# Kernel optimization log

Measured on AMD Instinct MI355X. Metric: run time of the kernel, lower is better.

Reference implementation:

```python
import jax, jax.numpy as jnp
import numpy as np

IN_DIM = 32000   # source vocab
OUT_DIM = 32000  # target vocab
HID = 1024
MAXLEN = 32      # decode steps
B = 64
SRC_LEN = 256


def _lstm_bias(h):
    # Keras LSTM: unit_forget_bias=True -> forget-gate bias = 1, rest 0. Gate order i,f,g,o.
    return jnp.concatenate([jnp.zeros(h), jnp.ones(h), jnp.zeros(2 * h)])


def setup_inputs() -> dict:
    key = jax.random.key(0)
    ks = jax.random.split(key, 12)
    g = lambda k, shape, s=0.02: (jax.random.normal(k, shape, jnp.float32) * s)
    return {
        "source": jax.random.randint(ks[0], (B, SRC_LEN), 0, IN_DIM, jnp.int32),
        "enc_emb": g(ks[1], (IN_DIM, HID)),
        "enc_K": g(ks[2], (HID, 4 * HID)),
        "enc_R": g(ks[3], (HID, 4 * HID)),
        "enc_b": _lstm_bias(HID),
        "dec_emb": g(ks[4], (OUT_DIM, HID)),
        "dec_K": g(ks[5], (HID, 4 * HID)),
        "dec_R": g(ks[6], (HID, 4 * HID)),
        "dec_b": _lstm_bias(HID),
        "W_a": g(ks[7], (HID, HID)),
        "W_c": g(ks[8], (2 * HID, HID)),
        "b_c": jnp.zeros(HID, jnp.float32),
        "W_out": g(ks[9], (HID, OUT_DIM)),
        "b_out": jnp.zeros(OUT_DIM, jnp.float32),
    }


def _lstm_cell(x, h, c, K, R, b):
    z = x @ K + h @ R + b
    i, f, g, o = jnp.split(z, 4, axis=-1)
    c = jax.nn.sigmoid(f) * c + jax.nn.sigmoid(i) * jnp.tanh(g)
    h = jax.nn.sigmoid(o) * jnp.tanh(c)
    return h, c


def reference(source, enc_emb, enc_K, enc_R, enc_b,
              dec_emb, dec_K, dec_R, dec_b,
              W_a, W_c, b_c, W_out, b_out):
    bsz = source.shape[0]
    hid = enc_K.shape[0]

    # ----- Encoder (mask_zero=True: skip state update where source==0) -----
    xe = enc_emb[source]                      # [B,T,H]
    mask = source > 0                         # [B,T]

    def enc_step(carry, xm):
        h, c = carry
        x, m = xm                             # x [B,H], m [B]
        hn, cn = _lstm_cell(x, h, c, enc_K, enc_R, enc_b)
        m = m[:, None]
        return (jnp.where(m, hn, h), jnp.where(m, cn, c)), jnp.where(m, hn, h)

    h0 = jnp.zeros((bsz, hid), xe.dtype)
    (he, ce), hs_t = jax.lax.scan(enc_step, (h0, h0),
                                  (xe.transpose(1, 0, 2), mask.T))
    hs = hs_t.transpose(1, 0, 2)              # [B,T,H] encoder states

    # ----- Decoder loop (greedy argmax feedback) -----
    hsW = hs @ W_a                            # [B,T,H], precomputed attention keys
    amask = mask[:, None, :].astype(hs.dtype)  # [B,1,T]

    def dec_step(carry, _):
        y, h, c = carry                       # y [B] int32
        x = dec_emb[y]                        # [B,H]
        hn, cn = _lstm_cell(x, h, c, dec_K, dec_R, dec_b)
        ht = hn[:, None, :]                   # [B,1,H]
        # Luong attention with source mask (exp -> mask -> normalize, as in source)
        sc = jnp.einsum('bqh,bkh->bqk', ht, hsW)        # [B,1,T]
        sc = jnp.exp(sc - sc.max(-1, keepdims=True)) * amask
        a = sc / sc.sum(-1, keepdims=True)
        ctx = jnp.einsum('bqk,bkh->bqh', a, hs)          # [B,1,H]
        ah = jnp.tanh(jnp.concatenate([ctx, ht], -1) @ W_c + b_c)
        prob = jax.nn.softmax(ah @ W_out + b_out, axis=-1)[:, 0, :]  # [B,V]
        yn = jnp.argmax(prob, axis=-1).astype(jnp.int32)
        return (yn, hn, cn), prob

    y0 = jnp.ones((bsz,), jnp.int32)          # start token = 1 (tf.ones)
    _, outs = jax.lax.scan(dec_step, (y0, he, ce), None, length=MAXLEN)
    return outs.transpose(1, 0, 2)            # [B, MAXLEN, OUT_DIM]
```

## Files before the change

### kernel.cpp

```cpp
#include <hip/hip_runtime.h>
#include <hip/hip_bf16.h>

typedef __hip_bfloat16 bf16;
typedef short bf8v __attribute__((ext_vector_type(8)));
typedef float f32x4 __attribute__((ext_vector_type(4)));

#define DEVINL __device__ __forceinline__
#define MFMA16(a, b, c) __builtin_amdgcn_mfma_f32_16x16x32_bf16((a), (b), (c), 0, 0, 0)

DEVINL float us2f(unsigned short u) { unsigned v = ((unsigned)u) << 16; return __uint_as_float(v); }
DEVINL float b2f(bf16 x) { return __bfloat162float(x); }
DEVINL bf16 f2b(float x) { return __float2bfloat16(x); }
DEVINL float sigf(float x) { return 1.0f / (1.0f + expf(-x)); }
DEVINL unsigned short f2bu(float f) { bf16 h = __float2bfloat16(f); return *(unsigned short*)&h; }

DEVINL void gload16(const void* g, void* l) {
  __builtin_amdgcn_global_load_lds((const __attribute__((address_space(1))) void*)g,
                                   (__attribute__((address_space(3))) void*)l, 16, 0, 0);
}

DEVINL unsigned ald(const unsigned* p) {
  return __hip_atomic_load(p, __ATOMIC_RELAXED, __HIP_MEMORY_SCOPE_AGENT);
}
DEVINL void ast(unsigned* p, unsigned v) {
  __hip_atomic_store(p, v, __ATOMIC_RELAXED, __HIP_MEMORY_SCOPE_AGENT);
}
DEVINL float aldf(const float* p) { unsigned u = ald((const unsigned*)p); return __uint_as_float(u); }
DEVINL void astf(float* p, float v) { ast((unsigned*)p, __float_as_uint(v)); }

DEVINL void gridbar2(unsigned* bars, unsigned lgen) {
  __syncthreads();
  if (threadIdx.x == 0) {
    unsigned s = lgen & 1;
    unsigned g = blockIdx.x >> 5;
    unsigned* grp = bars + (g * 2 + s) * 16;
    unsigned* top = bars + (16 + s) * 16;
    unsigned* gen = bars + 288;
    unsigned t = __hip_atomic_fetch_add(grp, 1u, __ATOMIC_RELAXED, __HIP_MEMORY_SCOPE_AGENT);
    if (t == 31u) {
      ast(grp, 0u);
      unsigned tt = __hip_atomic_fetch_add(top, 1u, __ATOMIC_RELAXED, __HIP_MEMORY_SCOPE_AGENT);
      if (tt == 7u) {
        ast(top, 0u);
        asm volatile("s_waitcnt vmcnt(0)");
        ast(gen, lgen + 1u);
      }
    }
    while (ald(gen) <= lgen) __builtin_amdgcn_s_sleep(4);
  }
  __syncthreads();
}

DEVINL void bar64(unsigned* b, unsigned lgen, int lid) {
  __syncthreads();
  if (threadIdx.x == 0) {
    unsigned s = lgen & 1;
    unsigned* grp = b + (((unsigned)(lid >> 5) & 1u) * 2 + s) * 16;
    unsigned* top = b + (4 + s) * 16;
    unsigned* gen = b + 96;
    unsigned t = __hip_atomic_fetch_add(grp, 1u, __ATOMIC_RELAXED, __HIP_MEMORY_SCOPE_AGENT);
    if (t == 31u) {
      ast(grp, 0u);
      unsigned tt = __hip_atomic_fetch_add(top, 1u, __ATOMIC_RELAXED, __HIP_MEMORY_SCOPE_AGENT);
      if (tt == 1u) {
        ast(top, 0u);
        asm volatile("s_waitcnt vmcnt(0)");
        ast(gen, lgen + 1u);
      }
    }
    while (ald(gen) <= lgen) __builtin_amdgcn_s_sleep(2);
  }
  __syncthreads();
}

#define OKPT_H  ((size_t)0)
#define OKPT_L  ((size_t)8388608)
#define ORPT_H  ((size_t)16777216)
#define ORPT_L  ((size_t)25165824)
#define OXE_H   ((size_t)35651584)
#define OXE_L   ((size_t)69206016)
#define OHSF5   ((size_t)35651584)
#define XCH     ((size_t)136314880)
#define OHPK_E0 (XCH + 0)
#define OHPK_E1 (XCH + 262144)
#define OHPK_D0 (XCH + 524288)
#define OCBUF5  (XCH + 1048576)
#define OAHPK   (XCH + 1310720)
#define ORSUM5  (XCH + 1572864)
#define ORMAX5  (XCH + 1638400)
#define ORIDX5  (XCH + 1769472)
#define OPSUM5  (XCH + 1900544)
#define OBARS5  (XCH + 1901568)
#define OXK_L5  ((size_t)138412032)
#define OWCT_H  ((size_t)0)
#define OWCT_L  ((size_t)4194304)
#define OPCTX5  ((size_t)8388608)
#define OQBUF   ORPT_H
#define OWOT5   ((size_t)138412032)
#define OKRTH5  ((size_t)203948032)
#define OKRTL5  ((size_t)220725248)

#define DELTA   1e-4f

#define D_LH   0
#define D_LL   32768
#define D_ZS   65536
#define D_KBH  83968
#define D_KBL  116736
#define D4_A   0
#define D4_W   16384
#define D4_E   49152
#define D_QL   0
#define D_PSC  4096
#define D_EK   8448
#define D_PC4  8704
#define D_ZS3  0
#define D_PSC2 0
#define D_GMX  4352
#define D_CCN  8512
#define D_CAND 8576
#define D_YL   149504
#define D_INV  149568
#define D_RT   149632

__global__ void ed_zero_v7(float4* p, int n) {
  int i = blockIdx.x * 256 + threadIdx.x;
  if (i < n) p[i] = make_float4(0.f, 0.f, 0.f, 0.f);
}

__global__ void ed_transpose_v7(const float* __restrict__ in, bf16* __restrict__ out,
                                int R, int C, int ostride, int ooff, int perm) {
  __shared__ float tile[32][33];
  int c0 = blockIdx.x * 32, r0 = blockIdx.y * 32;
  int tx = threadIdx.x & 31, ty0 = threadIdx.x >> 5;
#pragma unroll
  for (int i = 0; i < 4; i++) {
    int ty = ty0 + i * 8;
    tile[ty][tx] = in[(size_t)(r0 + ty) * C + c0 + tx];
  }
  __syncthreads();
#pragma unroll
  for (int i = 0; i < 4; i++) {
    int ty = ty0 + i * 8;
    int c = c0 + ty;
    int oc = perm ? ((c & 1023) * 4 + (c >> 10)) : c;
    out[(size_t)oc * ostride + ooff + r0 + tx] = f2b(tile[tx][ty]);
  }
}

__global__ void ed_transpose_split_v7(const float* __restrict__ in, bf16* __restrict__ oh,
                                      bf16* __restrict__ ol, int R, int C, int ostride,
                                      int ooff, int perm) {
  __shared__ float tile[32][33];
  int c0 = blockIdx.x * 32, r0 = blockIdx.y * 32;
  int tx = threadIdx.x & 31, ty0 = threadIdx.x >> 5;
#pragma unroll
  for (int i = 0; i < 4; i++) {
    int ty = ty0 + i * 8;
    tile[ty][tx] = in[(size_t)(r0 + ty) * C + c0 + tx];
  }
  __syncthreads();
#pragma unroll
  for (int i = 0; i < 4; i++) {
    int ty = ty0 + i * 8;
    int c = c0 + ty;
    int oc = perm ? ((c & 1023) * 4 + (c >> 10)) : c;
    float v = tile[tx][ty];
    bf16 hh = f2b(v);
    size_t o = (size_t)oc * ostride + ooff + r0 + tx;
    oh[o] = hh;
    ol[o] = f2b(v - b2f(hh));
  }
}

__global__ void ed_gather_split_v7(const int* __restrict__ src, const float* __restrict__ emb,
                                   bf16* __restrict__ xh, bf16* __restrict__ xl) {
  int bid = blockIdx.x;
  int t = bid >> 6, b = bid & 63;
  int tok = src[b * 256 + t];
  const float* rowp = emb + (size_t)tok * 1024;
  int i = threadIdx.x * 4;
  float4 v = *(const float4*)(rowp + i);
  bf16 h0 = f2b(v.x), h1 = f2b(v.y), h2 = f2b(v.z), h3 = f2b(v.w);
  ushort4 oh, ol;
  oh.x = *(unsigned short*)&h0; oh.y = *(unsigned short*)&h1;
  oh.z = *(unsigned short*)&h2; oh.w = *(unsigned short*)&h3;
  ol.x = f2bu(v.x - b2f(h0)); ol.y = f2bu(v.y - b2f(h1));
  ol.z = f2bu(v.z - b2f(h2)); ol.w = f2bu(v.w - b2f(h3));
  *(ushort4*)(xh + (size_t)bid * 1024 + i) = oh;
  *(ushort4*)(xl + (size_t)bid * 1024 + i) = ol;
}

__global__ __launch_bounds__(256, 2) void ed_gemm3_v7(
    const bf16* __restrict__ Ah, const bf16* __restrict__ Al,
    const bf16* __restrict__ Bh, const bf16* __restrict__ Bl,
    bf16* __restrict__ Ch, bf16* __restrict__ Cl, int M, int N, int K) {
  __shared__ __align__(16) bf16 Ash[128 * 32];
  __shared__ __align__(16) bf16 Asl[128 * 32];
  __shared__ __align__(16) bf16 Bsh[128 * 32];
  __shared__ __align__(16) bf16 Bsl[128 * 32];
  int m0 = blockIdx.y * 128, n0 = blockIdx.x * 128;
  int tid = threadIdx.x, w = tid >> 6, l = tid & 63;
  int wm = w >> 1, wn = w & 1;
  int lr = l & 15, lq = l >> 4;
  f32x4 acc[4][4] = {};
  for (int k0 = 0; k0 < K; k0 += 32) {
    __syncthreads();
#pragma unroll
    for (int j = 0; j < 2; j++) {
      int o = (w * 2 + j) * 1024 + l * 16;
      int rrow = o >> 6, kk = (o & 63) >> 1;
      gload16(Ah + (size_t)(m0 + rrow) * K + k0 + kk, (char*)Ash + (w * 2 + j) * 1024);
      gload16(Al + (size_t)(m0 + rrow) * K + k0 + kk, (char*)Asl + (w * 2 + j) * 1024);
      gload16(Bh + (size_t)(n0 + rrow) * K + k0 + kk, (char*)Bsh + (w * 2 + j) * 1024);
      gload16(Bl + (size_t)(n0 + rrow) * K + k0 + kk, (char*)Bsl + (w * 2 + j) * 1024);
    }
    __syncthreads();
#pragma unroll
    for (int mi = 0; mi < 4; mi++) {
      bf8v a_h = *(const bf8v*)(Ash + (wm * 64 + mi * 16 + lr) * 32 + lq * 8);
      bf8v a_l = *(const bf8v*)(Asl + (wm * 64 + mi * 16 + lr) * 32 + lq * 8);
#pragma unroll
      for (int ni = 0; ni < 4; ni++) {
        bf8v b_h = *(const bf8v*)(Bsh + (wn * 64 + ni * 16 + lr) * 32 + lq * 8);
        bf8v b_l = *(const bf8v*)(Bsl + (wn * 64 + ni * 16 + lr) * 32 + lq * 8);
        acc[mi][ni] = MFMA16(a_h, b_h, acc[mi][ni]);
        acc[mi][ni] = MFMA16(a_h, b_l, acc[mi][ni]);
        acc[mi][ni] = MFMA16(a_l, b_h, acc[mi][ni]);
      }
    }
  }
#pragma unroll
  for (int mi = 0; mi < 4; mi++)
#pragma unroll
    for (int ni = 0; ni < 4; ni++)
#pragma unroll
      for (int r = 0; r < 4; r++) {
        float v = acc[mi][ni][r];
        bf16 hh = f2b(v);
        size_t idx = (size_t)(m0 + wm * 64 + mi * 16 + lq * 4 + r) * N + n0 + wn * 64 + ni * 16 + lr;
        Ch[idx] = hh;
        Cl[idx] = f2b(v - b2f(hh));
      }
}

__global__ __launch_bounds__(1024, 4) void ed_enc_v7(
    const int* __restrict__ src, const bf16* __restrict__ Rh, const bf16* __restrict__ Rl,
    const bf16* __restrict__ Xh, const bf16* __restrict__ Xl, const float* __restrict__ enc_b,
    unsigned* hpk0, unsigned* hpk1, float* __restrict__ cbuf,
    float* __restrict__ hsf, unsigned* barsE) {
  extern __shared__ char sm[];
  bf16* lh = (bf16*)sm;
  bf16* ll = (bf16*)(sm + 32768);
  float* zs = (float*)(sm + 65536);
  float* xkf = (float*)(sm + 82944);
  int bid = blockIdx.x, tid = threadIdx.x;
  int bg = bid >> 6, cg = bid & 63, lid = bid & 63;
  unsigned* barL = barsE + bg * 128;
  int wv = tid >> 6, l = tid & 63, lr = l & 15, lq = l >> 4;
  int kq = wv >> 2, cs = wv & 3;
  int srow = tid >> 6, sj0 = (tid & 63) * 16;
  int grow = tid >> 4, gul = tid & 15;
  bf8v Rh_[8], Rl_[8];
  {
    const bf16* bh = Rh + (size_t)(cg * 64 + cs * 16 + lr) * 1024 + kq * 256 + lq * 8;
    const bf16* bl = Rl + (size_t)(cg * 64 + cs * 16 + lr) * 1024 + kq * 256 + lq * 8;
#pragma unroll
    for (int i = 0; i < 8; i++) {
      Rh_[i] = *(const bf8v*)(bh + i * 32);
      Rl_[i] = *(const bf8v*)(bl + i * 32);
    }
  }
  float bi[4];
  float c_ = 0.f;
  if (tid < 256) {
#pragma unroll
    for (int g = 0; g < 4; g++) {
      int colp = cg * 64 + gul * 4 + g;
      bi[g] = enc_b[(colp & 3) * 1024 + (colp >> 2)];
    }
  }
  unsigned *hc = hpk0, *hn = hpk1;
  unsigned lgen = 0;
  for (int t = 0; t < 256; t++) {
    {
      const unsigned* hrow = hc + (size_t)(bg * 16 + srow) * 1024 + sj0;
      unsigned u[16];
#pragma unroll
      for (int j = 0; j < 16; j++) u[j] = ald(hrow + j);
      int r8 = (srow & 7) << 3;
#pragma unroll
      for (int j = 0; j < 16; j += 2) {
        int es = (sj0 + j) ^ r8;
        *(unsigned*)((char*)lh + srow * 2048 + es * 2) = (u[j] >> 16) | (u[j + 1] & 0xffff0000u);
        *(unsigned*)((char*)ll + srow * 2048 + es * 2) = (u[j] & 0xffffu) | (u[j + 1] << 16);
      }
    }
    {
      int xr = tid >> 6, xc = tid & 63;
      size_t xi = ((size_t)t * 64 + bg * 16 + xr) * 4096 + cg * 64 + xc;
      unsigned short xh = __builtin_nontemporal_load((const unsigned short*)(Xh + xi));
      unsigned short xl = __builtin_nontemporal_load((const unsigned short*)(Xl + xi));
      xkf[xr * 64 + xc] = us2f(xh) + us2f(xl);
    }
    __syncthreads();
    {
      f32x4 acc = {0.f, 0.f, 0.f, 0.f};
      int r8 = (lr & 7) << 3;
#pragma unroll
      for (int i = 0; i < 8; i++) {
        int e0 = kq * 256 + i * 32 + lq * 8;
        int es = e0 ^ r8;
        bf8v a_h = *(const bf8v*)((char*)lh + lr * 2048 + es * 2);
        bf8v a_l = *(const bf8v*)((char*)ll + lr * 2048 + es * 2);
        acc = MFMA16(a_h, Rh_[i], acc);
        acc = MFMA16(a_h, Rl_[i], acc);
        acc = MFMA16(a_l, Rh_[i], acc);
        acc = MFMA16(a_l, Rl_[i], acc);
      }
#pragma unroll
      for (int r = 0; r < 4; r++) zs[(kq * 16 + lq * 4 + r) * 68 + cs * 16 + lr] = acc[r];
    }
    __syncthreads();
    if (tid < 256) {
      int b_ = bg * 16 + grow, u = cg * 16 + gul;
      float zz[4];
#pragma unroll
      for (int g = 0; g < 4; g++) {
        int cc = gul * 4 + g;
        zz[g] = zs[(0 + grow) * 68 + cc] + zs[(16 + grow) * 68 + cc] +
                zs[(32 + grow) * 68 + cc] + zs[(48 + grow) * 68 + cc] +
                xkf[grow * 64 + cc] + bi[g];
      }
      float iv = sigf(zz[0]), fv = sigf(zz[1]), gv = tanhf(zz[2]), ov = sigf(zz[3]);
      float cn = fv * c_ + iv * gv;
      float hnv = ov * tanhf(cn);
      bool m = src[b_ * 256 + t] > 0;
      int es = u ^ ((grow & 7) << 3);
      float hold = b2f(*(const bf16*)((char*)lh + grow * 2048 + es * 2)) +
                   b2f(*(const bf16*)((char*)ll + grow * 2048 + es * 2));
      float hv = m ? hnv : hold;
      c_ = m ? cn : c_;
      unsigned short uh = f2bu(hv);
      unsigned pkv = ((unsigned)uh << 16) | (unsigned)f2bu(hv - us2f(uh));
      ast(hn + (size_t)b_ * 1024 + u, pkv);
      hsf[((size_t)t * 64 + b_) * 1024 + u] = hv;
    }
    bar64(barL, lgen, lid);
    lgen++;
    unsigned* tp = hc; hc = hn; hn = tp;
  }
  if (tid < 256) cbuf[(size_t)(bg * 16 + grow) * 1024 + cg * 16 + gul] = c_;
}

DEVINL void dec_lstm7(int bg, int cgl, int tid, char* sm,
                      const unsigned* hc, unsigned* hn,
                      const float* __restrict__ dec_emb,
                      const bf16* __restrict__ Kh, const bf16* __restrict__ Kl,
                      const float* __restrict__ dec_b, float& c_) {
  bf16* lh = (bf16*)(sm + D_LH);
  bf16* ll = (bf16*)(sm + D_LL);
  {
    int srow = tid >> 6, sl = tid & 63;
    const unsigned* hrow = hc + (size_t)(bg * 16 + srow) * 1024 + sl * 16;
    unsigned u[16];
#pragma unroll
    for (int j = 0; j < 16; j++) u[j] = ald(hrow + j);
    uint4 ha, hb, la, lb;
    ha.x = (u[0] >> 16) | (u[1] & 0xffff0000u);  ha.y = (u[2] >> 16) | (u[3] & 0xffff0000u);
    ha.z = (u[4] >> 16) | (u[5] & 0xffff0000u);  ha.w = (u[6] >> 16) | (u[7] & 0xffff0000u);
    hb.x = (u[8] >> 16) | (u[9] & 0xffff0000u);  hb.y = (u[10] >> 16) | (u[11] & 0xffff0000u);
    hb.z = (u[12] >> 16) | (u[13] & 0xffff0000u); hb.w = (u[14] >> 16) | (u[15] & 0xffff0000u);
    la.x = (u[0] & 0xffffu) | (u[1] << 16);  la.y = (u[2] & 0xffffu) | (u[3] << 16);
    la.z = (u[4] & 0xffffu) | (u[5] << 16);  la.w = (u[6] & 0xffffu) | (u[7] << 16);
    lb.x = (u[8] & 0xffffu) | (u[9] << 16);  lb.y = (u[10] & 0xffffu) | (u[11] << 16);
    lb.z = (u[12] & 0xffffu) | (u[13] << 16); lb.w = (u[14] & 0xffffu) | (u[15] << 16);
    int swz = (srow & 7) << 4;
    char* rbh = (char*)lh + srow * 2048;
    char* rbl = (char*)ll + srow * 2048;
    *(uint4*)(rbh + ((sl * 32) ^ swz)) = ha;
    *(uint4*)(rbh + ((sl * 32 + 16) ^ swz)) = hb;
    *(uint4*)(rbl + ((sl * 32) ^ swz)) = la;
    *(uint4*)(rbl + ((sl * 32 + 16) ^ swz)) = lb;
  }
  int wv = tid >> 6, l = tid & 63, lr = l & 15, lq = l >> 4;
  int kg2 = wv >> 2, cs = wv & 3;
  bf16* kbh = (bf16*)(sm + D_KBH);
  bf16* kbl = (bf16*)(sm + D_KBL);
  const int* y_l = (const int*)(sm + D_YL);
  float* zs = (float*)(sm + D_ZS);
  f32x4 acc = {0.f, 0.f, 0.f, 0.f};
  int colB = cs * 16 + lr;
  int bswz = (colB & 7) << 4;
  int aswz = (lr & 7) << 4;
  for (int c = 0; c < 8; c++) {
    __syncthreads();
#pragma unroll
    for (int r = 0; r < 2; r++) {
      int i = wv * 128 + r * 64 + l;
      int col = i >> 5, j = i & 31;
      size_t se = (size_t)(cgl * 64 + col) * 2048 + c * 256 + ((size_t)(j ^ (col & 7)) << 3);
      gload16(Kh + se, (char*)kbh + wv * 2048 + r * 1024);
      gload16(Kl + se, (char*)kbl + wv * 2048 + r * 1024);
    }
    __syncthreads();
#pragma unroll
    for (int s = 0; s < 2; s++) {
      int kl = kg2 * 64 + s * 32 + lq * 8;
      bf8v b_h = *(const bf8v*)((char*)kbh + colB * 512 + ((kl * 2) ^ bswz));
      bf8v b_l = *(const bf8v*)((char*)kbl + colB * 512 + ((kl * 2) ^ bswz));
      int gk = c * 256 + kl;
      bf8v a_h, a_l;
      if (gk < 1024) {
        const float* xr = dec_emb + (size_t)y_l[lr] * 1024 + gk;
        float4 v0 = *(const float4*)xr;
        float4 v1 = *(const float4*)(xr + 4);
        float vs[8] = {v0.x, v0.y, v0.z, v0.w, v1.x, v1.y, v1.z, v1.w};
#pragma unroll
        for (int e = 0; e < 8; e++) {
          unsigned short uh = f2bu(vs[e]);
          a_h[e] = (short)uh;
          a_l[e] = (short)f2bu(vs[e] - us2f(uh));
        }
      } else {
        int hk = gk - 1024;
        a_h = *(const bf8v*)((char*)lh + lr * 2048 + ((hk * 2) ^ aswz));
        a_l = *(const bf8v*)((char*)ll + lr * 2048 + ((hk * 2) ^ aswz));
      }
      acc = MFMA16(a_h, b_h, acc);
      acc = MFMA16(a_h, b_l, acc);
      acc = MFMA16(a_l, b_h, acc);
      acc = MFMA16(a_l, b_l, acc);
    }
  }
#pragma unroll
  for (int r = 0; r < 4; r++) zs[(kg2 * 16 + lq * 4 + r) * 68 + cs * 16 + lr] = acc[r];
  __syncthreads();
  if (tid < 256) {
    int grow = tid >> 4, gul = tid & 15;
    int b_ = bg * 16 + grow;
    float zz[4];
#pragma unroll
    for (int g = 0; g < 4; g++) {
      int cc = gul * 4 + g;
      int colp = cgl * 64 + cc;
      float v = zs[(0 + grow) * 68 + cc] + zs[(16 + grow) * 68 + cc] +
                zs[(32 + grow) * 68 + cc] + zs[(48 + grow) * 68 + cc];
      zz[g] = v + dec_b[(colp & 3) * 1024 + (colp >> 2)];
    }
    float iv = sigf(zz[0]), fv = sigf(zz[1]), gv = tanhf(zz[2]), ov = sigf(zz[3]);
    float cn = fv * c_ + iv * gv;
    c_ = cn;
    float hv = ov * tanhf(cn);
    unsigned short uh = f2bu(hv);
    unsigned pkv = ((unsigned)uh << 16) | (unsigned)f2bu(hv - us2f(uh));
    ast(hn + (size_t)b_ * 1024 + cgl * 16 + gul, pkv);
  }
}

__global__ __launch_bounds__(1024, 4) void ed_dec_v7(
    const int* __restrict__ src,
    const bf16* __restrict__ KRh, const bf16* __restrict__ KRl, const float* __restrict__ dec_b,
    const bf16* __restrict__ WcTh, const bf16* __restrict__ WcTl, const float* __restrict__ b_cp,
    const bf16* __restrict__ WoTh, const float* __restrict__ b_op,
    const float* __restrict__ Wout_f32, const float* __restrict__ dec_emb,
    const float* __restrict__ W_a, float* __restrict__ qbuf,
    const float* __restrict__ hsf,
    unsigned* hpkA, unsigned* hpkB, float* __restrict__ cbuf,
    float* __restrict__ pctx, float* __restrict__ psum, unsigned* ahpk,
    float* __restrict__ rowsum, float* __restrict__ rmax, int* __restrict__ ridx,
    float* __restrict__ out, unsigned* barsG, unsigned* barsL) {
  extern __shared__ char sm[];
  int bid = blockIdx.x, tid = threadIdx.x;
  int bg = bid >> 6, cgl = bid & 63, lid = bid & 63;
  unsigned* barL = barsL + bg * 128;
  int wv = tid >> 6, l = tid & 63, lr = l & 15, lq = l >> 4;
  float c_ = 0.f;
  if (tid < 256) c_ = cbuf[(size_t)(bg * 16 + (tid >> 4)) * 1024 + cgl * 16 + (tid & 15)];
  unsigned *hc = hpkA, *hn = hpkB;
  unsigned lgenL = 0, lgenG = 0;

  if (tid < 16) ((int*)(sm + D_YL))[tid] = 1;
  __syncthreads();
  dec_lstm7(bg, cgl, tid, sm, hc, hn, dec_emb, KRh, KRl, dec_b, c_);
  bar64(barL, lgenL, lid); lgenL++;
  { unsigned* tp = hc; hc = hn; hn = tp; }

  for (int st = 0; st < 32; st++) {
    if (cgl < 16) {
      int colb = cgl * 64;
      int kq = wv >> 2, nq = wv & 3;
      float* zs = (float*)(sm + D_ZS);
      f32x4 acc = {0.f, 0.f, 0.f, 0.f};
      const unsigned* hrow = hc + (size_t)(bg * 16 + lr) * 1024;
      const float* warow = W_a + (size_t)(colb + nq * 16 + lr) * 1024;
#pragma unroll
      for (int i = 0; i < 8; i++) {
        int k = kq * 256 + i * 32 + lq * 8;
        bf8v a, b;
        const unsigned* hp = hrow + k;
#pragma unroll
        for (int e = 0; e < 8; e++) a[e] = (short)(ald(hp + e) >> 16);
        const float* wp = warow + k;
        float4 w0 = *(const float4*)wp;
        float4 w1 = *(const float4*)(wp + 4);
        b[0] = (short)f2bu(w0.x); b[1] = (short)f2bu(w0.y);
        b[2] = (short)f2bu(w0.z); b[3] = (short)f2bu(w0.w);
        b[4] = (short)f2bu(w1.x); b[5] = (short)f2bu(w1.y);
        b[6] = (short)f2bu(w1.z); b[7] = (short)f2bu(w1.w);
        acc = MFMA16(a, b, acc);
      }
#pragma unroll
      for (int r = 0; r < 4; r++) zs[(kq * 16 + lq * 4 + r) * 68 + nq * 16 + lr] = acc[r];
      __syncthreads();
      {
        int mrow = tid >> 6, col = tid & 63;
        float v = zs[(0 + mrow) * 68 + col] + zs[(16 + mrow) * 68 + col] +
                  zs[(32 + mrow) * 68 + col] + zs[(48 + mrow) * 68 + col];
        astf(qbuf + (size_t)(bg * 16 + mrow) * 1024 + colb + col, v);
      }
    }
    bar64(barL, lgenL, lid); lgenL++;
    {
      int b_ = bid >> 2, kg = bid & 3;
      float* q_l = (float*)(sm + D_QL);
      q_l[tid] = aldf(qbuf + (size_t)b_ * 1024 + tid);
      __syncthreads();
      float* psc = (float*)(sm + D_PSC);
      {
        int kl = tid >> 4, qq = tid & 15;
        const float* hrow = hsf + ((size_t)(kg * 64 + kl) * 64 + b_) * 1024;
        float p = 0.f;
#pragma unroll 4
        for (int j = 0; j < 16; j++) {
          int e0 = j * 64 + qq * 4;
          float4 hv = *(const float4*)(hrow + e0);
          p += hv.x * q_l[e0] + hv.y * q_l[e0 + 1] + hv.z * q_l[e0 + 2] + hv.w * q_l[e0 + 3];
        }
        psc[kl * 17 + qq] = p;
      }
      __syncthreads();
      float* ek = (float*)(sm + D_EK);
      if (tid < 64) {
        float sc = 0.f;
#pragma unroll
        for (int q = 0; q < 16; q++) sc += psc[tid * 17 + q];
        ek[tid] = (src[b_ * 256 + kg * 64 + tid] > 0) ? expf(sc) : 0.f;
      }
      __syncthreads();
      float* pc4 = (float*)(sm + D_PC4);
      {
        int cq = tid & 255, kc = tid >> 8;
        float a0 = 0.f, a1 = 0.f, a2 = 0.f, a3 = 0.f;
#pragma unroll 4
        for (int j = 0; j < 16; j++) {
          float e = ek[kc * 16 + j];
          const float* hr = hsf + ((size_t)(kg * 64 + kc * 16 + j) * 64 + b_) * 1024 + cq * 4;
          float4 uv = *(const float4*)hr;
          a0 += e * uv.x; a1 += e * uv.y; a2 += e * uv.z; a3 += e * uv.w;
        }
        pc4[kc * 1024 + cq * 4 + 0] = a0;
        pc4[kc * 1024 + cq * 4 + 1] = a1;
        pc4[kc * 1024 + cq * 4 + 2] = a2;
        pc4[kc * 1024 + cq * 4 + 3] = a3;
      }
      __syncthreads();
      {
        float v = pc4[tid] + pc4[1024 + tid] + pc4[2048 + tid] + pc4[3072 + tid];
        astf(pctx + ((size_t)kg * 64 + b_) * 1024 + tid, v);
      }
      if (tid == 0) {
        float* ek2 = (float*)(sm + D_EK);
        float s_ = 0.f;
        for (int i2 = 0; i2 < 64; i2++) s_ += ek2[i2];
        astf(psum + kg * 64 + b_, s_);
      }
    }
    bar64(barL, lgenL, lid); lgenL++;
    {
      float* inv_l = (float*)(sm + D_INV);
      if (tid < 16) {
        int rb = bg * 16 + tid;
        float sg = aldf(psum + rb) + aldf(psum + 64 + rb) +
                   aldf(psum + 128 + rb) + aldf(psum + 192 + rb);
        inv_l[tid] = 1.0f / sg;
      }
      __syncthreads();
      float* zs3 = (float*)(sm + D_ZS3);
      {
        int kq = wv;
        f32x4 acc = {0.f, 0.f, 0.f, 0.f};
        const bf16* bh = WcTh + (size_t)(cgl * 16 + lr) * 2048;
        const bf16* bl = WcTl + (size_t)(cgl * 16 + lr) * 2048;
        float inv = inv_l[lr];
#pragma unroll
        for (int i = 0; i < 4; i++) {
          int k = kq * 128 + i * 32 + lq * 8;
          bf8v a_h, a_l;
          if (k < 1024) {
            const float* p0 = pctx + (size_t)(bg * 16 + lr) * 1024 + k;
#pragma unroll
            for (int e = 0; e < 8; e++) {
              float v = (aldf(p0 + e) + aldf(p0 + 65536 + e) +
                         aldf(p0 + 131072 + e) + aldf(p0 + 196608 + e)) * inv;
              unsigned short uh = f2bu(v);
              a_h[e] = (short)uh;
              a_l[e] = (short)f2bu(v - us2f(uh));
            }
          } else {
            const unsigned* hp = hc + (size_t)(bg * 16 + lr) * 1024 + (k - 1024);
#pragma unroll
            for (int e = 0; e < 8; e++) {
              unsigned u = ald(hp + e);
              a_h[e] = (short)(u >> 16);
              a_l[e] = (short)(u & 0xffffu);
            }
          }
          bf8v b_h = *(const bf8v*)(bh + k);
          bf8v b_l = *(const bf8v*)(bl + k);
          acc = MFMA16(a_h, b_h, acc); acc = MFMA16(a_h, b_l, acc);
          acc = MFMA16(a_l, b_h, acc); acc = MFMA16(a_l, b_l, acc);
        }
#pragma unroll
        for (int r = 0; r < 4; r++) zs3[(kq * 16 + lq * 4 + r) * 17 + lr] = acc[r];
      }
      __syncthreads();
      if (tid < 256) {
        int grow = tid >> 4, gcol = tid & 15;
        float v = 0.f;
#pragma unroll
        for (int q = 0; q < 16; q++) v += zs3[(q * 16 + grow) * 17 + gcol];
        v += b_cp[cgl * 16 + gcol];
        float ahv = tanhf(v);
        unsigned short uh = f2bu(ahv);
        unsigned pkv = ((unsigned)uh << 16) | (unsigned)f2bu(ahv - us2f(uh));
        ast(ahpk + (size_t)(bg * 16 + grow) * 1024 + cgl * 16 + gcol, pkv);
      }
    }
    gridbar2(barsG, lgenG); lgenG++;
    {
      int base = bid * 125;
      bf16* abuf = (bf16*)(sm + D4_A);
      bf16* wbuf = (bf16*)(sm + D4_W);
      int rg = wv >> 2, cpair = wv & 3;
      f32x4 acc0 = {0.f, 0.f, 0.f, 0.f}, acc1 = {0.f, 0.f, 0.f, 0.f};
      for (int kc = 0; kc < 8; kc++) {
        int k0 = kc * 128;
        __syncthreads();
        {
          int row = tid >> 4, l16 = tid & 15;
          const unsigned* ap = ahpk + (size_t)row * 1024 + k0 + l16 * 8;
          unsigned u0 = ald(ap), u1 = ald(ap + 1), u2 = ald(ap + 2), u3 = ald(ap + 3);
          unsigned u4 = ald(ap + 4), u5 = ald(ap + 5), u6 = ald(ap + 6), u7 = ald(ap + 7);
          uint4 hv;
          hv.x = (u0 >> 16) | (u1 & 0xffff0000u);
          hv.y = (u2 >> 16) | (u3 & 0xffff0000u);
          hv.z = (u4 >> 16) | (u5 & 0xffff0000u);
          hv.w = (u6 >> 16) | (u7 & 0xffff0000u);
          *(uint4*)((char*)abuf + row * 256 + ((l16 * 16) ^ ((row & 7) << 4))) = hv;
        }
#pragma unroll
        for (int r = 0; r < 2; r++) {
          int i = wv * 128 + r * 64 + l;
          int col = i >> 4, j = i & 15;
          int ccol = col < 125 ? col : 124;
          size_t se = (size_t)(base + ccol) * 1024 + k0 + ((size_t)(j ^ (col & 7)) << 3);
          gload16(WoTh + se, (char*)wbuf + wv * 2048 + r * 1024);
        }
        __syncthreads();
#pragma unroll
        for (int s = 0; s < 4; s++) {
          int kl = s * 32 + lq * 8;
          int ar = rg * 16 + lr;
          bf8v a = *(const bf8v*)((char*)abuf + ar * 256 + ((kl * 2) ^ ((ar & 7) << 4)));
          int c0 = cpair * 32 + lr, c1 = c0 + 16;
          bf8v b0 = *(const bf8v*)((char*)wbuf + c0 * 256 + ((kl * 2) ^ ((c0 & 7) << 4)));
          bf8v b1 = *(const bf8v*)((char*)wbuf + c1 * 256 + ((kl * 2) ^ ((c1 & 7) << 4)));
          acc0 = MFMA16(a, b0, acc0);
          acc1 = MFMA16(a, b1, acc1);
        }
      }
      __syncthreads();
      float* e = (float*)(sm + D4_E);
      {
        int cl0 = cpair * 32 + lr;
        if (cl0 < 125) {
#pragma unroll
          for (int r = 0; r < 4; r++)
            e[(rg * 16 + lq * 4 + r) * 129 + cl0] = acc0[r] + b_op[base + cl0];
        }
        int cl1 = cpair * 32 + 16 + lr;
        if (cl1 < 125) {
#pragma unroll
          for (int r = 0; r < 4; r++)
            e[(rg * 16 + lq * 4 + r) * 129 + cl1] = acc1[r] + b_op[base + cl1];
        }
      }
      __syncthreads();
      if (tid < 64) {
        float sm_ = 0.f, v1 = -1e30f, v2 = -1e30f;
        int i1 = 0, i2 = 0;
        for (int c2 = 0; c2 < 125; c2++) {
          float v = e[tid * 129 + c2];
          sm_ += expf(v);
          if (v > v1) { v2 = v1; i2 = i1; v1 = v; i1 = base + c2; }
          else if (v > v2) { v2 = v; i2 = base + c2; }
        }
        astf(rowsum + bid * 64 + tid, sm_);
        astf(rmax + (bid * 64 + tid) * 2 + 0, v1);
        ast((unsigned*)ridx + (bid * 64 + tid) * 2 + 0, (unsigned)i1);
        astf(rmax + (bid * 64 + tid) * 2 + 1, v2);
        ast((unsigned*)ridx + (bid * 64 + tid) * 2 + 1, (unsigned)i2);
      }
    }
    gridbar2(barsG, lgenG); lgenG++;
    {
      float* psc2 = (float*)(sm + D_PSC2);
      {
        int rr = tid & 63, pp = tid >> 6;
        float s_ = 0.f;
#pragma unroll 4
        for (int cu = pp * 16; cu < pp * 16 + 16; cu++) s_ += aldf(rowsum + cu * 64 + rr);
        psc2[rr * 17 + pp] = s_;
      }
      __syncthreads();
      float* rt = (float*)(sm + D_RT);
      if (tid < 64) {
        float s_ = 0.f;
#pragma unroll
        for (int p2 = 0; p2 < 16; p2++) s_ += psc2[tid * 17 + p2];
        rt[tid] = s_;
      }
      __syncthreads();
      float* e = (float*)(sm + D4_E);
      {
        int base = bid * 125;
        for (int i = tid; i < 8000; i += 1024) {
          int r_ = i / 125, c2 = i - r_ * 125;
          float pv = expf(e[r_ * 129 + c2]) / rt[r_];
          __builtin_nontemporal_store(pv, out + ((size_t)r_ * 32 + st) * 32000 + base + c2);
        }
      }
      if (st < 31) {
        float* gmx = (float*)(sm + D_GMX);
        int* ccnt = (int*)(sm + D_CCN);
        int* cand = (int*)(sm + D_CAND);
        int* y_l = (int*)(sm + D_YL);
        int r16 = tid & 15, ch = tid >> 4;
        int rowg = bg * 16 + r16;
        float vloc[8]; int iloc[8];
        {
          float m_ = -1e30f;
#pragma unroll
          for (int ee = 0; ee < 8; ee++) {
            int ent = ch * 8 + ee;
            vloc[ee] = aldf(rmax + ((size_t)(ent >> 1) * 64 + rowg) * 2 + (ent & 1));
            iloc[ee] = (int)ald((const unsigned*)ridx + ((size_t)(ent >> 1) * 64 + rowg) * 2 + (ent & 1));
            m_ = fmaxf(m_, vloc[ee]);
          }
          gmx[r16 * 65 + ch] = m_;
        }
        if (tid < 16) ccnt[tid] = 0;
        __syncthreads();
        if (tid < 16) {
          float g_ = -1e30f;
#pragma unroll
          for (int j = 0; j < 64; j++) g_ = fmaxf(g_, gmx[tid * 65 + j]);
          gmx[tid * 65 + 64] = g_;
        }
        __syncthreads();
        {
          float thr = gmx[r16 * 65 + 64] - DELTA;
#pragma unroll
          for (int ee = 0; ee < 8; ee++) {
            if (vloc[ee] >= thr) {
              int slot = atomicAdd(&ccnt[r16], 1);
              if (slot < 8) cand[r16 * 8 + slot] = iloc[ee];
            }
          }
        }
        __syncthreads();
        {
          int row2 = wv;
          int rowg2 = bg * 16 + row2;
          int cnt = ccnt[row2]; if (cnt > 8) cnt = 8;
          double bv = -1e30; int bi_ = 0x7fffffff;
          for (int ci = 0; ci < cnt; ci++) {
            int c = cand[row2 * 8 + ci];
            double s_ = 0.0;
            for (int k = l; k < 1024; k += 64) {
              unsigned u = ald(ahpk + (size_t)rowg2 * 1024 + k);
              float av = us2f((unsigned short)(u >> 16)) + us2f((unsigned short)(u & 0xffffu));
              float wv_ = __builtin_nontemporal_load(Wout_f32 + (size_t)k * 32000 + c);
              s_ += (double)av * (double)wv_;
            }
#pragma unroll
            for (int off = 32; off > 0; off >>= 1) s_ += __shfl_down(s_, off);
            if (l == 0) {
              s_ += (double)b_op[c];
              if (s_ > bv || (s_ == bv && c < bi_)) { bv = s_; bi_ = c; }
            }
          }
          if (l == 0) y_l[row2] = bi_;
        }
        __syncthreads();
        dec_lstm7(bg, cgl, tid, sm, hc, hn, dec_emb, KRh, KRl, dec_b, c_);
      }
    }
    bar64(barL, lgenL, lid); lgenL++;
    { unsigned* tp = hc; hc = hn; hn = tp; }
  }
}

extern "C" void kernel_launch(void* const* d_in, const int* in_sizes, int n_in,
                              void* d_out, int out_size, void* d_ws, size_t ws_size,
                              hipStream_t stream) {
  (void)in_sizes; (void)n_in; (void)out_size; (void)ws_size;
  const int*   src     = (const int*)  d_in[0];
  const float* enc_emb = (const float*)d_in[1];
  const float* enc_K   = (const float*)d_in[2];
  const float* enc_R   = (const float*)d_in[3];
  const float* enc_b   = (const float*)d_in[4];
  const float* dec_emb = (const float*)d_in[5];
  const float* dec_K   = (const float*)d_in[6];
  const float* dec_R   = (const float*)d_in[7];
  const float* dec_b   = (const float*)d_in[8];
  const float* W_a     = (const float*)d_in[9];
  const float* W_c     = (const float*)d_in[10];
  const float* b_c     = (const float*)d_in[11];
  const float* W_out   = (const float*)d_in[12];
  const float* b_out   = (const float*)d_in[13];
  char* ws = (char*)d_ws;

  hipFuncSetAttribute((const void*)ed_enc_v7, hipFuncAttributeMaxDynamicSharedMemorySize, 163840);
  hipFuncSetAttribute((const void*)ed_dec_v7, hipFuncAttributeMaxDynamicSharedMemorySize, 163840);

  bf16* KpTh = (bf16*)(ws + OKPT_H);
  bf16* KpTl = (bf16*)(ws + OKPT_L);
  bf16* RpTh = (bf16*)(ws + ORPT_H);
  bf16* RpTl = (bf16*)(ws + ORPT_L);
  bf16* xeh  = (bf16*)(ws + OXE_H);
  bf16* xel  = (bf16*)(ws + OXE_L);
  float* hsf = (float*)(ws + OHSF5);
  unsigned* hpkE0 = (unsigned*)(ws + OHPK_E0);
  unsigned* hpkE1 = (unsigned*)(ws + OHPK_E1);
  unsigned* hpkD0 = (unsigned*)(ws + OHPK_D0);
  float* cbuf = (float*)(ws + OCBUF5);
  unsigned* ahpk = (unsigned*)(ws + OAHPK);
  float* rsum = (float*)(ws + ORSUM5);
  float* rmaxp = (float*)(ws + ORMAX5);
  int*  ridxp = (int*)(ws + ORIDX5);
  float* psum = (float*)(ws + OPSUM5);
  unsigned* barsE = (unsigned*)(ws + OBARS5);
  unsigned* barsG = (unsigned*)(ws + OBARS5 + 4096);
  unsigned* barsL = (unsigned*)(ws + OBARS5 + 8192);
  bf16* XkL  = (bf16*)(ws + OXK_L5);
  bf16* XkH  = (bf16*)d_out;
  bf16* WcTh = (bf16*)(ws + OWCT_H);
  bf16* WcTl = (bf16*)(ws + OWCT_L);
  float* pctx = (float*)(ws + OPCTX5);
  float* qbuf = (float*)(ws + OQBUF);
  bf16* WoTh = (bf16*)(ws + OWOT5);
  bf16* KRTh = (bf16*)(ws + OKRTH5);
  bf16* KRTl = (bf16*)(ws + OKRTL5);

  ed_zero_v7<<<512, 256, 0, stream>>>((float4*)(ws + XCH), 131072);
  ed_transpose_split_v7<<<dim3(128, 32), 256, 0, stream>>>(enc_K, KpTh, KpTl, 1024, 4096, 1024, 0, 1);
  ed_transpose_split_v7<<<dim3(128, 32), 256, 0, stream>>>(enc_R, RpTh, RpTl, 1024, 4096, 1024, 0, 1);
  ed_gather_split_v7<<<16384, 256, 0, stream>>>(src, enc_emb, xeh, xel);
  ed_gemm3_v7<<<dim3(32, 128), 256, 0, stream>>>(xeh, xel, KpTh, KpTl, XkH, XkL, 16384, 4096, 1024);
  ed_transpose_split_v7<<<dim3(32, 64), 256, 0, stream>>>(W_c, WcTh, WcTl, 2048, 1024, 2048, 0, 0);
  ed_enc_v7<<<256, 1024, 87040, stream>>>(src, RpTh, RpTl, XkH, XkL, enc_b,
                                          hpkE0, hpkE1, cbuf, hsf, barsE);
  ed_transpose_v7<<<dim3(1000, 32), 256, 0, stream>>>(W_out, WoTh, 1024, 32000, 1024, 0, 0);
  ed_transpose_split_v7<<<dim3(128, 32), 256, 0, stream>>>(dec_K, KRTh, KRTl, 1024, 4096, 2048, 0, 1);
  ed_transpose_split_v7<<<dim3(128, 32), 256, 0, stream>>>(dec_R, KRTh, KRTl, 1024, 4096, 2048, 1024, 1);
  ed_dec_v7<<<256, 1024, 150528, stream>>>(src, KRTh, KRTl, dec_b, WcTh, WcTl, b_c,
                                           WoTh, b_out, W_out, dec_emb, W_a, qbuf, hsf,
                                           hpkE0, hpkD0, cbuf, pctx, psum, ahpk,
                                           rsum, rmaxp, ridxp, (float*)d_out, barsG, barsL);
}
```

Measured before the change: 14.43 ms.

## Restructure decoder attention, argmax reduction, and pre-convert W_a to bf16

```diff
diff --git a/kernel.cpp b/kernel.cpp
--- a/kernel.cpp
+++ b/kernel.cpp
@@ -91,11 +91,13 @@
 #define ORIDX5  (XCH + 1769472)
 #define OPSUM5  (XCH + 1900544)
 #define OBARS5  (XCH + 1901568)
+#define OYBUF   (XCH + 1917952)
 #define OXK_L5  ((size_t)138412032)
 #define OWCT_H  ((size_t)0)
 #define OWCT_L  ((size_t)4194304)
 #define OPCTX5  ((size_t)8388608)
 #define OQBUF   ORPT_H
+#define OWAB    (ORPT_H + 262144)
 #define OWOT5   ((size_t)138412032)
 #define OKRTH5  ((size_t)203948032)
 #define OKRTL5  ((size_t)220725248)
@@ -110,25 +112,36 @@
 #define D4_A   0
 #define D4_W   16384
 #define D4_E   49152
-#define D_QL   0
-#define D_PSC  4096
-#define D_EK   8448
-#define D_PC4  8704
+#define D_WA   0
+#define D_ES   65536
 #define D_ZS3  0
 #define D_PSC2 0
-#define D_GMX  4352
-#define D_CCN  8512
-#define D_CAND 8576
+#define D_RV   0
+#define D_RR   2048
+#define D_CCN  4096
+#define D_CAND 4160
+#define D_RS   4224
+#define D_RC   4352
 #define D_YL   149504
 #define D_INV  149568
 #define D_RT   149632
 
-__global__ void ed_zero_v7(float4* p, int n) {
+__global__ void ed_zero_v8(float4* p, int n) {
   int i = blockIdx.x * 256 + threadIdx.x;
   if (i < n) p[i] = make_float4(0.f, 0.f, 0.f, 0.f);
 }
 
-__global__ void ed_transpose_v7(const float* __restrict__ in, bf16* __restrict__ out,
+__global__ void ed_cvt_v8(const float* __restrict__ in, bf16* __restrict__ out, int n) {
+  int i = (blockIdx.x * 256 + threadIdx.x) * 4;
+  if (i + 3 < n) {
+    float4 v = *(const float4*)(in + i);
+    ushort4 o;
+    o.x = f2bu(v.x); o.y = f2bu(v.y); o.z = f2bu(v.z); o.w = f2bu(v.w);
+    *(ushort4*)(out + i) = o;
+  }
+}
+
+__global__ void ed_transpose_v8(const float* __restrict__ in, bf16* __restrict__ out,
                                 int R, int C, int ostride, int ooff, int perm) {
   __shared__ float tile[32][33];
   int c0 = blockIdx.x * 32, r0 = blockIdx.y * 32;
@@ -148,7 +161,7 @@
   }
 }
 
-__global__ void ed_transpose_split_v7(const float* __restrict__ in, bf16* __restrict__ oh,
+__global__ void ed_transpose_split_v8(const float* __restrict__ in, bf16* __restrict__ oh,
                                       bf16* __restrict__ ol, int R, int C, int ostride,
                                       int ooff, int perm) {
   __shared__ float tile[32][33];
@@ -173,7 +186,7 @@
   }
 }
 
-__global__ void ed_gather_split_v7(const int* __restrict__ src, const float* __restrict__ emb,
+__global__ void ed_gather_split_v8(const int* __restrict__ src, const float* __restrict__ emb,
                                    bf16* __restrict__ xh, bf16* __restrict__ xl) {
   int bid = blockIdx.x;
   int t = bid >> 6, b = bid & 63;
@@ -191,7 +204,7 @@
   *(ushort4*)(xl + (size_t)bid * 1024 + i) = ol;
 }
 
-__global__ __launch_bounds__(256, 2) void ed_gemm3_v7(
+__global__ __launch_bounds__(256, 2) void ed_gemm3_v8(
     const bf16* __restrict__ Ah, const bf16* __restrict__ Al,
     const bf16* __restrict__ Bh, const bf16* __restrict__ Bl,
     bf16* __restrict__ Ch, bf16* __restrict__ Cl, int M, int N, int K) {
@@ -244,7 +257,7 @@
       }
 }
 
-__global__ __launch_bounds__(1024, 4) void ed_enc_v7(
+__global__ __launch_bounds__(1024, 4) void ed_enc_v8(
     const int* __restrict__ src, const bf16* __restrict__ Rh, const bf16* __restrict__ Rl,
     const bf16* __restrict__ Xh, const bf16* __restrict__ Xl, const float* __restrict__ enc_b,
     unsigned* hpk0, unsigned* hpk1, float* __restrict__ cbuf,
@@ -353,7 +366,7 @@
   if (tid < 256) cbuf[(size_t)(bg * 16 + grow) * 1024 + cg * 16 + gul] = c_;
 }
 
-DEVINL void dec_lstm7(int bg, int cgl, int tid, char* sm,
+DEVINL void dec_lstm8(int bg, int cgl, int tid, char* sm,
                       const unsigned* hc, unsigned* hn,
                       const float* __restrict__ dec_emb,
                       const bf16* __restrict__ Kh, const bf16* __restrict__ Kl,
@@ -458,18 +471,18 @@
   }
 }
 
-__global__ __launch_bounds__(1024, 4) void ed_dec_v7(
+__global__ __launch_bounds__(1024, 4) void ed_dec_v8(
     const int* __restrict__ src,
     const bf16* __restrict__ KRh, const bf16* __restrict__ KRl, const float* __restrict__ dec_b,
     const bf16* __restrict__ WcTh, const bf16* __restrict__ WcTl, const float* __restrict__ b_cp,
     const bf16* __restrict__ WoTh, const float* __restrict__ b_op,
     const float* __restrict__ Wout_f32, const float* __restrict__ dec_emb,
-    const float* __restrict__ W_a, float* __restrict__ qbuf,
+    const bf16* __restrict__ WaB, float* __restrict__ qbuf,
     const float* __restrict__ hsf,
     unsigned* hpkA, unsigned* hpkB, float* __restrict__ cbuf,
     float* __restrict__ pctx, float* __restrict__ psum, unsigned* ahpk,
     float* __restrict__ rowsum, float* __restrict__ rmax, int* __restrict__ ridx,
-    float* __restrict__ out, unsigned* barsG, unsigned* barsL) {
+    unsigned* ybuf, float* __restrict__ out, unsigned* barsG, unsigned* barsL) {
   extern __shared__ char sm[];
   int bid = blockIdx.x, tid = threadIdx.x;
   int bg = bid >> 6, cgl = bid & 63, lid = bid & 63;
@@ -482,7 +495,7 @@
 
   if (tid < 16) ((int*)(sm + D_YL))[tid] = 1;
   __syncthreads();
-  dec_lstm7(bg, cgl, tid, sm, hc, hn, dec_emb, KRh, KRl, dec_b, c_);
+  dec_lstm8(bg, cgl, tid, sm, hc, hn, dec_emb, KRh, KRl, dec_b, c_);
   bar64(barL, lgenL, lid); lgenL++;
   { unsigned* tp = hc; hc = hn; hn = tp; }
 
@@ -493,21 +506,15 @@
       float* zs = (float*)(sm + D_ZS);
       f32x4 acc = {0.f, 0.f, 0.f, 0.f};
       const unsigned* hrow = hc + (size_t)(bg * 16 + lr) * 1024;
-      const float* warow = W_a + (size_t)(colb + nq * 16 + lr) * 1024;
+      const bf16* warow = WaB + (size_t)(colb + nq * 16 + lr) * 1024;
 #pragma unroll
       for (int i = 0; i < 8; i++) {
         int k = kq * 256 + i * 32 + lq * 8;
-        bf8v a, b;
+        bf8v a;
         const unsigned* hp = hrow + k;
 #pragma unroll
         for (int e = 0; e < 8; e++) a[e] = (short)(ald(hp + e) >> 16);
-        const float* wp = warow + k;
-        float4 w0 = *(const float4*)wp;
-        float4 w1 = *(const float4*)(wp + 4);
-        b[0] = (short)f2bu(w0.x); b[1] = (short)f2bu(w0.y);
-        b[2] = (short)f2bu(w0.z); b[3] = (short)f2bu(w0.w);
-        b[4] = (short)f2bu(w1.x); b[5] = (short)f2bu(w1.y);
-        b[6] = (short)f2bu(w1.z); b[7] = (short)f2bu(w1.w);
+        bf8v b = *(const bf8v*)(warow + k);
         acc = MFMA16(a, b, acc);
       }
 #pragma unroll
@@ -523,56 +530,55 @@
     bar64(barL, lgenL, lid); lgenL++;
     {
       int b_ = bid >> 2, kg = bid & 3;
-      float* q_l = (float*)(sm + D_QL);
-      q_l[tid] = aldf(qbuf + (size_t)b_ * 1024 + tid);
-      __syncthreads();
-      float* psc = (float*)(sm + D_PSC);
+      float* wacc = (float*)(sm + D_WA);
+      float* es = (float*)(sm + D_ES);
+      float qr[16];
       {
-        int kl = tid >> 4, qq = tid & 15;
-        const float* hrow = hsf + ((size_t)(kg * 64 + kl) * 64 + b_) * 1024;
+        const float* qb = qbuf + (size_t)b_ * 1024 + l * 16;
+        *(float4*)&qr[0]  = *(const float4*)(qb);
+        *(float4*)&qr[4]  = *(const float4*)(qb + 4);
+        *(float4*)&qr[8]  = *(const float4*)(qb + 8);
+        *(float4*)&qr[12] = *(const float4*)(qb + 12);
+      }
+      float a16[16];
+#pragma unroll
+      for (int j = 0; j < 16; j++) a16[j] = 0.f;
+      float esum = 0.f;
+#pragma unroll
+      for (int i = 0; i < 4; i++) {
+        int kglob = kg * 64 + wv * 4 + i;
+        const float* hrow = hsf + ((size_t)kglob * 64 + b_) * 1024 + l * 16;
+        float4 v0 = *(const float4*)hrow;
+        float4 v1 = *(const float4*)(hrow + 4);
+        float4 v2 = *(const float4*)(hrow + 8);
+        float4 v3 = *(const float4*)(hrow + 12);
+        float vv[16] = {v0.x, v0.y, v0.z, v0.w, v1.x, v1.y, v1.z, v1.w,
+                        v2.x, v2.y, v2.z, v2.w, v3.x, v3.y, v3.z, v3.w};
         float p = 0.f;
-#pragma unroll 4
-        for (int j = 0; j < 16; j++) {
-          int e0 = j * 64 + qq * 4;
-          float4 hv = *(const float4*)(hrow + e0);
-          p += hv.x * q_l[e0] + hv.y * q_l[e0 + 1] + hv.z * q_l[e0 + 2] + hv.w * q_l[e0 + 3];
-        }
-        psc[kl * 17 + qq] = p;
-      }
-      __syncthreads();
-      float* ek = (float*)(sm + D_EK);
-      if (tid < 64) {
-        float sc = 0.f;
-#pragma unroll
-        for (int q = 0; q < 16; q++) sc += psc[tid * 17 + q];
-        ek[tid] = (src[b_ * 256 + kg * 64 + tid] > 0) ? expf(sc) : 0.f;
-      }
-      __syncthreads();
-      float* pc4 = (float*)(sm + D_PC4);
-      {
-        int cq = tid & 255, kc = tid >> 8;
-        float a0 = 0.f, a1 = 0.f, a2 = 0.f, a3 = 0.f;
-#pragma unroll 4
-        for (int j = 0; j < 16; j++) {
-          float e = ek[kc * 16 + j];
-          const float* hr = hsf + ((size_t)(kg * 64 + kc * 16 + j) * 64 + b_) * 1024 + cq * 4;
-          float4 uv = *(const float4*)hr;
-          a0 += e * uv.x; a1 += e * uv.y; a2 += e * uv.z; a3 += e * uv.w;
-        }
-        pc4[kc * 1024 + cq * 4 + 0] = a0;
-        pc4[kc * 1024 + cq * 4 + 1] = a1;
-        pc4[kc * 1024 + cq * 4 + 2] = a2;
-        pc4[kc * 1024 + cq * 4 + 3] = a3;
-      }
+#pragma unroll
+        for (int j = 0; j < 16; j++) p += qr[j] * vv[j];
+#pragma unroll
+        for (int off = 32; off > 0; off >>= 1) p += __shfl_xor(p, off);
+        float e = (src[b_ * 256 + kglob] > 0) ? expf(p) : 0.f;
+        esum += e;
+#pragma unroll
+        for (int j = 0; j < 16; j++) a16[j] += e * vv[j];
+      }
+#pragma unroll
+      for (int j = 0; j < 16; j++) wacc[wv * 1024 + j * 64 + l] = a16[j];
+      if (l == 0) es[wv] = esum;
       __syncthreads();
       {
-        float v = pc4[tid] + pc4[1024 + tid] + pc4[2048 + tid] + pc4[3072 + tid];
-        astf(pctx + ((size_t)kg * 64 + b_) * 1024 + tid, v);
+        float v = 0.f;
+#pragma unroll
+        for (int w2 = 0; w2 < 16; w2++) v += wacc[w2 * 1024 + tid];
+        int logical = (tid & 63) * 16 + (tid >> 6);
+        astf(pctx + ((size_t)kg * 64 + b_) * 1024 + logical, v);
       }
       if (tid == 0) {
-        float* ek2 = (float*)(sm + D_EK);
         float s_ = 0.f;
-        for (int i2 = 0; i2 < 64; i2++) s_ += ek2[i2];
+#pragma unroll
+        for (int w2 = 0; w2 < 16; w2++) s_ += es[w2];
         astf(psum + kg * 64 + b_, s_);
       }
     }
@@ -742,69 +748,62 @@
         }
       }
       if (st < 31) {
-        float* gmx = (float*)(sm + D_GMX);
-        int* ccnt = (int*)(sm + D_CCN);
-        int* cand = (int*)(sm + D_CAND);
         int* y_l = (int*)(sm + D_YL);
-        int r16 = tid & 15, ch = tid >> 4;
-        int rowg = bg * 16 + r16;
-        float vloc[8]; int iloc[8];
-        {
-          float m_ = -1e30f;
-#pragma unroll
-          for (int ee = 0; ee < 8; ee++) {
-            int ent = ch * 8 + ee;
-            vloc[ee] = aldf(rmax + ((size_t)(ent >> 1) * 64 + rowg) * 2 + (ent & 1));
-            iloc[ee] = (int)ald((const unsigned*)ridx + ((size_t)(ent >> 1) * 64 + rowg) * 2 + (ent & 1));
-            m_ = fmaxf(m_, vloc[ee]);
+        if (cgl < 16) {
+          int rowg = bg * 16 + cgl;
+          float* rv = (float*)(sm + D_RV);
+          float* rr2 = (float*)(sm + D_RR);
+          int* ccnt = (int*)(sm + D_CCN);
+          int* cand = (int*)(sm + D_CAND);
+          double* rs = (double*)(sm + D_RS);
+          int* rc = (int*)(sm + D_RC);
+          float myv = -1e30f;
+          if (tid < 512) {
+            myv = aldf(rmax + ((size_t)(tid >> 1) * 64 + rowg) * 2 + (tid & 1));
+            rv[tid] = myv;
+            rr2[tid] = myv;
           }
-          gmx[r16 * 65 + ch] = m_;
-        }
-        if (tid < 16) ccnt[tid] = 0;
-        __syncthreads();
-        if (tid < 16) {
-          float g_ = -1e30f;
-#pragma unroll
-          for (int j = 0; j < 64; j++) g_ = fmaxf(g_, gmx[tid * 65 + j]);
-          gmx[tid * 65 + 64] = g_;
-        }
-        __syncthreads();
-        {
-          float thr = gmx[r16 * 65 + 64] - DELTA;
-#pragma unroll
-          for (int ee = 0; ee < 8; ee++) {
-            if (vloc[ee] >= thr) {
-              int slot = atomicAdd(&ccnt[r16], 1);
-              if (slot < 8) cand[r16 * 8 + slot] = iloc[ee];
-            }
+          if (tid == 0) ccnt[0] = 0;
+          __syncthreads();
+          for (int w2 = 256; w2 >= 1; w2 >>= 1) {
+            if (tid < w2) rr2[tid] = fmaxf(rr2[tid], rr2[tid + w2]);
+            __syncthreads();
           }
-        }
-        __syncthreads();
-        {
-          int row2 = wv;
-          int rowg2 = bg * 16 + row2;
-          int cnt = ccnt[row2]; if (cnt > 8) cnt = 8;
-          double bv = -1e30; int bi_ = 0x7fffffff;
-          for (int ci = 0; ci < cnt; ci++) {
-            int c = cand[row2 * 8 + ci];
+          float thr = rr2[0] - DELTA;
+          if (tid < 512 && myv >= thr) {
+            int slot = atomicAdd(&ccnt[0], 1);
+            if (slot < 16)
+              cand[slot] = (int)ald((const unsigned*)ridx +
+                                    ((size_t)(tid >> 1) * 64 + rowg) * 2 + (tid & 1));
+          }
+          __syncthreads();
+          int cnt = ccnt[0] < 16 ? ccnt[0] : 16;
+          if (wv < cnt) {
+            int c = cand[wv];
             double s_ = 0.0;
             for (int k = l; k < 1024; k += 64) {
-              unsigned u = ald(ahpk + (size_t)rowg2 * 1024 + k);
+              unsigned u = ald(ahpk + (size_t)rowg * 1024 + k);
               float av = us2f((unsigned short)(u >> 16)) + us2f((unsigned short)(u & 0xffffu));
-              float wv_ = __builtin_nontemporal_load(Wout_f32 + (size_t)k * 32000 + c);
-              s_ += (double)av * (double)wv_;
+              s_ += (double)av * (double)Wout_f32[(size_t)k * 32000 + c];
             }
 #pragma unroll
             for (int off = 32; off > 0; off >>= 1) s_ += __shfl_down(s_, off);
-            if (l == 0) {
-              s_ += (double)b_op[c];
-              if (s_ > bv || (s_ == bv && c < bi_)) { bv = s_; bi_ = c; }
+            if (l == 0) { rs[wv] = s_ + (double)b_op[c]; rc[wv] = c; }
+          }
+          __syncthreads();
+          if (tid == 0) {
+            double bv = -1e30; int bc = 0x7fffffff;
+            for (int ci = 0; ci < cnt; ci++) {
+              double s_ = rs[ci]; int c = rc[ci];
+              if (s_ > bv || (s_ == bv && c < bc)) { bv = s_; bc = c; }
             }
+            ast(ybuf + rowg, (unsigned)bc);
           }
-          if (l == 0) y_l[row2] = bi_;
-        }
+        }
+        bar64(barL, lgenL, lid); lgenL++;
+        if (tid < 16) y_l[tid] = (int)ald(ybuf + bg * 16 + tid);
         __syncthreads();
-        dec_lstm7(bg, cgl, tid, sm, hc, hn, dec_emb, KRh, KRl, dec_b, c_);
+        dec_lstm8(bg, cgl, tid, sm, hc, hn, dec_emb, KRh, KRl, dec_b, c_);
       }
     }
     bar64(barL, lgenL, lid); lgenL++;
@@ -832,8 +831,8 @@
   const float* b_out   = (const float*)d_in[13];
   char* ws = (char*)d_ws;
 
-  hipFuncSetAttribute((const void*)ed_enc_v7, hipFuncAttributeMaxDynamicSharedMemorySize, 163840);
-  hipFuncSetAttribute((const void*)ed_dec_v7, hipFuncAttributeMaxDynamicSharedMemorySize, 163840);
+  hipFuncSetAttribute((const void*)ed_enc_v8, hipFuncAttributeMaxDynamicSharedMemorySize, 163840);
+  hipFuncSetAttribute((const void*)ed_dec_v8, hipFuncAttributeMaxDynamicSharedMemorySize, 163840);
 
   bf16* KpTh = (bf16*)(ws + OKPT_H);
   bf16* KpTl = (bf16*)(ws + OKPT_L);
@@ -854,29 +853,33 @@
   unsigned* barsE = (unsigned*)(ws + OBARS5);
   unsigned* barsG = (unsigned*)(ws + OBARS5 + 4096);
   unsigned* barsL = (unsigned*)(ws + OBARS5 + 8192);
+  unsigned* ybuf = (unsigned*)(ws + OYBUF);
   bf16* XkL  = (bf16*)(ws + OXK_L5);
   bf16* XkH  = (bf16*)d_out;
   bf16* WcTh = (bf16*)(ws + OWCT_H);
   bf16* WcTl = (bf16*)(ws + OWCT_L);
   float* pctx = (float*)(ws + OPCTX5);
   float* qbuf = (float*)(ws + OQBUF);
+  bf16* WaB  = (bf16*)(ws + OWAB);
   bf16* WoTh = (bf16*)(ws + OWOT5);
   bf16* KRTh = (bf16*)(ws + OKRTH5);
   bf16* KRTl = (bf16*)(ws + OKRTL5);
 
-  ed_zero_v7<<<512, 256, 0, stream>>>((float4*)(ws + XCH), 131072);
-  ed_transpose_split_v7<<<dim3(128, 32), 256, 0, stream>>>(enc_K, KpTh, KpTl, 1024, 4096, 1024, 0, 1);
-  ed_transpose_split_v7<<<dim3(128, 32), 256, 0, stream>>>(enc_R, RpTh, RpTl, 1024, 4096, 1024, 0, 1);
-  ed_gather_split_v7<<<16384, 256, 0, stream>>>(src, enc_emb, xeh, xel);
-  ed_gemm3_v7<<<dim3(32, 128), 256, 0, stream>>>(xeh, xel, KpTh, KpTl, XkH, XkL, 16384, 4096, 1024);
-  ed_transpose_split_v7<<<dim3(32, 64), 256, 0, stream>>>(W_c, WcTh, WcTl, 2048, 1024, 2048, 0, 0);
-  ed_enc_v7<<<256, 1024, 87040, stream>>>(src, RpTh, RpTl, XkH, XkL, enc_b,
+  ed_zero_v8<<<512, 256, 0, stream>>>((float4*)(ws + XCH), 131072);
+  ed_transpose_split_v8<<<dim3(128, 32), 256, 0, stream>>>(enc_K, KpTh, KpTl, 1024, 4096, 1024, 0, 1);
+  ed_transpose_split_v8<<<dim3(128, 32), 256, 0, stream>>>(enc_R, RpTh, RpTl, 1024, 4096, 1024, 0, 1);
+  ed_gather_split_v8<<<16384, 256, 0, stream>>>(src, enc_emb, xeh, xel);
+  ed_gemm3_v8<<<dim3(32, 128), 256, 0, stream>>>(xeh, xel, KpTh, KpTl, XkH, XkL, 16384, 4096, 1024);
+  ed_transpose_split_v8<<<dim3(32, 64), 256, 0, stream>>>(W_c, WcTh, WcTl, 2048, 1024, 2048, 0, 0);
+  ed_enc_v8<<<256, 1024, 87040, stream>>>(src, RpTh, RpTl, XkH, XkL, enc_b,
                                           hpkE0, hpkE1, cbuf, hsf, barsE);
-  ed_transpose_v7<<<dim3(1000, 32), 256, 0, stream>>>(W_out, WoTh, 1024, 32000, 1024, 0, 0);
-  ed_transpose_split_v7<<<dim3(128, 32), 256, 0, stream>>>(dec_K, KRTh, KRTl, 1024, 4096, 2048, 0, 1);
-  ed_transpose_split_v7<<<dim3(128, 32), 256, 0, stream>>>(dec_R, KRTh, KRTl, 1024, 4096, 2048, 1024, 1);
-  ed_dec_v7<<<256, 1024, 150528, stream>>>(src, KRTh, KRTl, dec_b, WcTh, WcTl, b_c,
-                                           WoTh, b_out, W_out, dec_emb, W_a, qbuf, hsf,
+  ed_cvt_v8<<<1024, 256, 0, stream>>>(W_a, WaB, 1048576);
+  ed_transpose_v8<<<dim3(1000, 32), 256, 0, stream>>>(W_out, WoTh, 1024, 32000, 1024, 0, 0);
+  ed_transpose_split_v8<<<dim3(128, 32), 256, 0, stream>>>(dec_K, KRTh, KRTl, 1024, 4096, 2048, 0, 1);
+  ed_transpose_split_v8<<<dim3(128, 32), 256, 0, stream>>>(dec_R, KRTh, KRTl, 1024, 4096, 2048, 1024, 1);
+  ed_dec_v8<<<256, 1024, 150528, stream>>>(src, KRTh, KRTl, dec_b, WcTh, WcTl, b_c,
+                                           WoTh, b_out, W_out, dec_emb, WaB, qbuf, hsf,
                                            hpkE0, hpkD0, cbuf, pctx, psum, ahpk,
-                                           rsum, rmaxp, ridxp, (float*)d_out, barsG, barsL);
-}
+                                           rsum, rmaxp, ridxp, ybuf, (float*)d_out,
+                                           barsG, barsL);
+}
```

Measured after the change: 12.43 ms. -13.8%, faster.
